# Kernel optimization log

Hardware: AMD Instinct MI355X
Metric: run time of the kernel (lower is better)

## Reference

```python
import jax, jax.numpy as jnp
import numpy as np

TOP_K = 2

def setup_inputs() -> dict:
    key = jax.random.key(0)
    ks = jax.random.split(key, 7)
    B, L, D, H, E, S = 2, 2048, 1024, 512, 16, 2048
    s = lambda fan_in: (1.0 / np.sqrt(fan_in)).astype(np.float32)
    return {
        "x": jax.random.normal(ks[0], (B, L, D), jnp.float32),
        "gate_w": jax.random.normal(ks[1], (E, D), jnp.float32) * s(D),
        "w1": jax.random.normal(ks[2], (E, H, D), jnp.float32) * s(D),
        "w2": jax.random.normal(ks[3], (E, D, H), jnp.float32) * s(H),
        "sfc1": jax.random.normal(ks[4], (S, D), jnp.float32) * s(D),
        "sfc2": jax.random.normal(ks[5], (S, D), jnp.float32) * s(D),
        "sfc3": jax.random.normal(ks[6], (D, S), jnp.float32) * s(S),
    }

def reference(x, gate_w, w1, w2, sfc1, sfc2, sfc3):
    B, L, D = x.shape
    E = gate_w.shape[0]
    # shared expert: SwiGLU MLP
    shared = jnp.einsum("bls,ds->bld", jax.nn.silu(jnp.einsum("bld,sd->bls", x, sfc1)) * jnp.einsum("bld,sd->bls", x, sfc2), sfc3)
    # router: top-k over gate logits, softmax over selected logits only
    logits = jnp.einsum("bld,ed->ble", x, gate_w)
    top_w, top_idx = jax.lax.top_k(logits, TOP_K)           # [B,L,K]
    top_w = jax.nn.softmax(top_w, axis=-1)
    xf = x.reshape(-1, D)                                    # [T,D]
    T = xf.shape[0]
    idx = top_idx.reshape(T, TOP_K)
    wk = top_w.reshape(T, TOP_K)
    # dense combine weights [T,E]: routing weight where selected, else 0
    dispatch = jnp.zeros((T, E), xf.dtype).at[jnp.arange(T)[:, None], idx].add(wk)
    # all-expert dense compute, combined with dispatch weights (avoids [T,E,D])
    h = jax.nn.silu(jnp.einsum("td,ehd->teh", xf, w1))       # [T,E,H]
    moe = jnp.einsum("teh,te,edh->td", h, dispatch, w2)      # [T,D]
    return moe.reshape(B, L, D) + shared
```

## Files before the change

kernel.cpp:

```cpp
#include <hip/hip_runtime.h>
#include <stdint.h>

#define T_TOK 4096
#define D_DIM 1024
#define H_DIM 512
#define E_NUM 16
#define S_DIM 2048

#define CAST2_BLOCKS 256
#define DUAL_BLOCKS 512
#define MOE1_TILES_MAX 80
#define SHOUT_BLOCKS 256

typedef __attribute__((ext_vector_type(8))) __bf16 bf16x8;
typedef __attribute__((ext_vector_type(4))) float f32x4;

__device__ __forceinline__ uint16_t f2bf(float f) {
  uint32_t u = __float_as_uint(f);
  u += 0x7fffu + ((u >> 16) & 1u);
  return (uint16_t)(u >> 16);
}

__device__ __forceinline__ float bf2f(uint16_t u) {
  return __uint_as_float(((uint32_t)u) << 16);
}

__device__ __forceinline__ float silu_f(float v) {
  return v / (1.f + __expf(-v));
}

#define N4_X (T_TOK * D_DIM / 4)
#define N4_S (S_DIM * D_DIM / 4)
#define N4_W (E_NUM * H_DIM * D_DIM / 4)
#define N4_P1 (N4_X + 2 * N4_S + N4_W)
#define N4_GW (E_NUM * D_DIM / 4)
#define N4_P2 (N4_S + N4_W)

__global__ __launch_bounds__(256) void k_cast1(
    const float* __restrict__ x, const float* __restrict__ sfc1,
    const float* __restrict__ sfc2, const float* __restrict__ w1,
    const float* __restrict__ gw,
    uint16_t* __restrict__ xb, uint16_t* __restrict__ s1b,
    uint16_t* __restrict__ s2b, uint16_t* __restrict__ w1b,
    float4* __restrict__ gwT4) {
  int i = blockIdx.x * 256 + threadIdx.x;
  if (i >= N4_P1) {
    int t = i - N4_P1;
    if (t < N4_GW) {
      int k4 = t & (D_DIM / 4 - 1);
      int e = t >> 8;
      gwT4[(size_t)k4 * E_NUM + e] = ((const float4*)(gw + (size_t)e * D_DIM))[k4];
    }
    return;
  }
  const float* src; uint16_t* dst; int off;
  if (i < N4_X)                  { src = x;    dst = xb;  off = 0; }
  else if (i < N4_X + N4_S)      { src = sfc1; dst = s1b; off = N4_X; }
  else if (i < N4_X + 2 * N4_S)  { src = sfc2; dst = s2b; off = N4_X + N4_S; }
  else                           { src = w1;   dst = w1b; off = N4_X + 2 * N4_S; }
  int j = i - off;
  float4 v = ((const float4*)src)[j];
  ushort4 o;
  o.x = f2bf(v.x); o.y = f2bf(v.y); o.z = f2bf(v.z); o.w = f2bf(v.w);
  ((ushort4*)dst)[j] = o;
}

__global__ __launch_bounds__(256) void k_router(
    const float* __restrict__ x, const float4* __restrict__ gwT4,
    int* __restrict__ top_idx, float* __restrict__ top_w) {
  const int wid = threadIdx.x >> 6, lane = threadIdx.x & 63;
  const int t = blockIdx.x * 4 + wid;
  const int e = lane & 15, q = lane >> 4;
  const float4* xr4 = (const float4*)(x + (size_t)t * D_DIM) + q * 64;
  const float4* g4 = gwT4 + (size_t)q * 64 * E_NUM + e;
  float acc = 0.f;
#pragma unroll 8
  for (int i = 0; i < 64; i++) {
    float4 xv = xr4[i];
    float4 gv = g4[(size_t)i * E_NUM];
    acc += xv.x * gv.x + xv.y * gv.y + xv.z * gv.z + xv.w * gv.w;
  }
  acc += __shfl_xor(acc, 16, 64);
  acc += __shfl_xor(acc, 32, 64);
  float v1 = acc; int i1 = e;
#pragma unroll
  for (int off = 1; off < 16; off <<= 1) {
    float ov = __shfl_xor(v1, off, 64);
    int oi = __shfl_xor(i1, off, 64);
    if (ov > v1 || (ov == v1 && oi < i1)) { v1 = ov; i1 = oi; }
  }
  float v2 = (e == i1) ? -1e30f : acc; int i2 = e;
#pragma unroll
  for (int off = 1; off < 16; off <<= 1) {
    float ov = __shfl_xor(v2, off, 64);
    int oi = __shfl_xor(i2, off, 64);
    if (ov > v2 || (ov == v2 && oi < i2)) { v2 = ov; i2 = oi; }
  }
  if (lane == 0) {
    float w0 = 1.f / (1.f + __expf(v2 - v1));
    top_idx[t * 2] = i1; top_idx[t * 2 + 1] = i2;
    top_w[t * 2] = w0;  top_w[t * 2 + 1] = 1.f - w0;
  }
}

__global__ __launch_bounds__(256) void k_sort(
    const int* __restrict__ top_idx, const float* __restrict__ top_w,
    int* __restrict__ offsets, int* __restrict__ tile_e,
    int* __restrict__ tile_m, int* __restrict__ tile_cnt,
    int* __restrict__ slot_token, float* __restrict__ slot_w,
    int* __restrict__ slot_of) {
  __shared__ int h[E_NUM];
  __shared__ int offs[E_NUM + 1];
  int tid = threadIdx.x;
  if (tid < E_NUM) h[tid] = 0;
  __syncthreads();
  for (int i = tid; i < 2 * T_TOK; i += 256) atomicAdd(&h[top_idx[i]], 1);
  __syncthreads();
  if (tid == 0) {
    int s = 0;
    for (int e = 0; e < E_NUM; e++) { offs[e] = s; s += h[e]; }
    offs[E_NUM] = s;
    int cnt = 0;
    for (int e = 0; e < E_NUM; e++)
      for (int m0 = 0; m0 < h[e]; m0 += 128) { tile_e[cnt] = e; tile_m[cnt] = m0; cnt++; }
    tile_cnt[0] = cnt;
    for (int e = 0; e <= E_NUM; e++) offsets[e] = offs[e];
  }
  __syncthreads();
  if (tid < E_NUM) h[tid] = offs[tid];
  __syncthreads();
  for (int i = tid; i < 2 * T_TOK; i += 256) {
    int e = top_idx[i];
    int slot = atomicAdd(&h[e], 1);
    slot_token[slot] = i >> 1;
    slot_w[slot] = top_w[i];
    slot_of[i] = slot;
  }
}

__global__ __launch_bounds__(256) void k_stage1(
    const uint16_t* __restrict__ xb, const uint16_t* __restrict__ b1,
    const uint16_t* __restrict__ b2, uint16_t* __restrict__ hs,
    const uint16_t* __restrict__ w1b, const int* __restrict__ offsets,
    const int* __restrict__ slot_token, const int* __restrict__ tile_e,
    const int* __restrict__ tile_m, const int* __restrict__ tile_cnt,
    uint16_t* __restrict__ hbuf,
    const float* __restrict__ sfc3, const float* __restrict__ w2,
    uint16_t* __restrict__ s3b, uint16_t* __restrict__ w2b) {
  __shared__ uint16_t smem[6 * 4096];
  const int bid = blockIdx.x;
  const int tid = threadIdx.x, lane = tid & 63, wid = tid >> 6;
  const int wm = wid >> 1, wn = wid & 1;
  const int r = lane & 15, q = lane >> 4;
  const int row0 = tid >> 2, col8 = (tid & 3) * 8;
  const int st0 = tid * 8, st1 = 2048 + tid * 8;

  if (bid < CAST2_BLOCKS) {
    for (int i = bid * 256 + tid; i < N4_P2; i += CAST2_BLOCKS * 256) {
      const float* src; uint16_t* dst; int j;
      if (i < N4_S) { src = sfc3; dst = s3b; j = i; }
      else          { src = w2;   dst = w2b; j = i - N4_S; }
      float4 v = ((const float4*)src)[j];
      ushort4 o;
      o.x = f2bf(v.x); o.y = f2bf(v.y); o.z = f2bf(v.z); o.w = f2bf(v.w);
      ((ushort4*)dst)[j] = o;
    }
    return;
  }

  if (bid < CAST2_BLOCKS + DUAL_BLOCKS) {
    const int b = bid - CAST2_BLOCKS;
    const int bm0 = (b & 31) * 128, bn0 = (b >> 5) * 128;
    uint16_t* sA = smem;
    uint16_t* sB1 = smem + 8192;
    uint16_t* sB2 = smem + 16384;
    f32x4 acc1[4][4], acc2[4][4];
#pragma unroll
    for (int i = 0; i < 4; i++)
#pragma unroll
      for (int j = 0; j < 4; j++) {
        acc1[i][j] = (f32x4){0.f, 0.f, 0.f, 0.f};
        acc2[i][j] = (f32x4){0.f, 0.f, 0.f, 0.f};
      }
    const uint16_t* ga0 = xb + (size_t)(bm0 + row0) * D_DIM + col8;
    const uint16_t* ga1 = ga0 + 64 * D_DIM;
    const uint16_t* gb10 = b1 + (size_t)(bn0 + row0) * D_DIM + col8;
    const uint16_t* gb11 = gb10 + 64 * D_DIM;
    const uint16_t* gb20 = b2 + (size_t)(bn0 + row0) * D_DIM + col8;
    const uint16_t* gb21 = gb20 + 64 * D_DIM;

    uint4 pA0, pA1, pB10, pB11, pB20, pB21;
    pA0 = *(const uint4*)ga0;   pA1 = *(const uint4*)ga1;
    pB10 = *(const uint4*)gb10; pB11 = *(const uint4*)gb11;
    pB20 = *(const uint4*)gb20; pB21 = *(const uint4*)gb21;
    ga0 += 32; ga1 += 32; gb10 += 32; gb11 += 32; gb20 += 32; gb21 += 32;
    *(uint4*)(sA + st0) = pA0;   *(uint4*)(sA + st1) = pA1;
    *(uint4*)(sB1 + st0) = pB10; *(uint4*)(sB1 + st1) = pB11;
    *(uint4*)(sB2 + st0) = pB20; *(uint4*)(sB2 + st1) = pB21;
    __syncthreads();

    int cur = 0;
    for (int kt = 32; kt < D_DIM; kt += 32) {
      pA0 = *(const uint4*)ga0;   pA1 = *(const uint4*)ga1;
      pB10 = *(const uint4*)gb10; pB11 = *(const uint4*)gb11;
      pB20 = *(const uint4*)gb20; pB21 = *(const uint4*)gb21;
      ga0 += 32; ga1 += 32; gb10 += 32; gb11 += 32; gb20 += 32; gb21 += 32;
      {
        const uint16_t* A = sA + cur * 4096;
        const uint16_t* B1 = sB1 + cur * 4096;
        const uint16_t* B2 = sB2 + cur * 4096;
        bf16x8 a[4];
#pragma unroll
        for (int i = 0; i < 4; i++)
          a[i] = *(const bf16x8*)(A + (wm * 64 + i * 16 + r) * 32 + q * 8);
#pragma unroll
        for (int j = 0; j < 4; j++) {
          bf16x8 b = *(const bf16x8*)(B1 + (wn * 64 + j * 16 + r) * 32 + q * 8);
#pragma unroll
          for (int i = 0; i < 4; i++)
            acc1[i][j] = __builtin_amdgcn_mfma_f32_16x16x32_bf16(a[i], b, acc1[i][j], 0, 0, 0);
        }
#pragma unroll
        for (int j = 0; j < 4; j++) {
          bf16x8 b = *(const bf16x8*)(B2 + (wn * 64 + j * 16 + r) * 32 + q * 8);
#pragma unroll
          for (int i = 0; i < 4; i++)
            acc2[i][j] = __builtin_amdgcn_mfma_f32_16x16x32_bf16(a[i], b, acc2[i][j], 0, 0, 0);
        }
      }
      int nxt = cur ^ 1;
      *(uint4*)(sA + nxt * 4096 + st0) = pA0;   *(uint4*)(sA + nxt * 4096 + st1) = pA1;
      *(uint4*)(sB1 + nxt * 4096 + st0) = pB10; *(uint4*)(sB1 + nxt * 4096 + st1) = pB11;
      *(uint4*)(sB2 + nxt * 4096 + st0) = pB20; *(uint4*)(sB2 + nxt * 4096 + st1) = pB21;
      __syncthreads();
      cur = nxt;
    }
    {
      const uint16_t* A = sA + cur * 4096;
      const uint16_t* B1 = sB1 + cur * 4096;
      const uint16_t* B2 = sB2 + cur * 4096;
      bf16x8 a[4];
#pragma unroll
      for (int i = 0; i < 4; i++)
        a[i] = *(const bf16x8*)(A + (wm * 64 + i * 16 + r) * 32 + q * 8);
#pragma unroll
      for (int j = 0; j < 4; j++) {
        bf16x8 b = *(const bf16x8*)(B1 + (wn * 64 + j * 16 + r) * 32 + q * 8);
#pragma unroll
        for (int i = 0; i < 4; i++)
          acc1[i][j] = __builtin_amdgcn_mfma_f32_16x16x32_bf16(a[i], b, acc1[i][j], 0, 0, 0);
      }
#pragma unroll
      for (int j = 0; j < 4; j++) {
        bf16x8 b = *(const bf16x8*)(B2 + (wn * 64 + j * 16 + r) * 32 + q * 8);
#pragma unroll
        for (int i = 0; i < 4; i++)
          acc2[i][j] = __builtin_amdgcn_mfma_f32_16x16x32_bf16(a[i], b, acc2[i][j], 0, 0, 0);
      }
    }
#pragma unroll
    for (int i = 0; i < 4; i++)
#pragma unroll
      for (int j = 0; j < 4; j++)
#pragma unroll
        for (int rr = 0; rr < 4; rr++) {
          int row = bm0 + wm * 64 + i * 16 + q * 4 + rr;
          int col = bn0 + wn * 64 + j * 16 + r;
          hs[(size_t)row * S_DIM + col] = f2bf(silu_f(acc1[i][j][rr]) * acc2[i][j][rr]);
        }
  } else {
    int idx = bid - CAST2_BLOCKS - DUAL_BLOCKS;
    int t = idx >> 2;
    if (t >= tile_cnt[0]) return;
    const int n0 = (idx & 3) * 128;
    const int e = tile_e[t], m0 = tile_m[t];
    const int base = offsets[e];
    const int ne = offsets[e + 1] - base;
    uint16_t* sA = smem;
    uint16_t* sB = smem + 8192;
    f32x4 acc[4][4];
#pragma unroll
    for (int i = 0; i < 4; i++)
#pragma unroll
      for (int j = 0; j < 4; j++) acc[i][j] = (f32x4){0.f, 0.f, 0.f, 0.f};
    const int e0 = min(m0 + row0, ne - 1);
    const int e1 = min(m0 + row0 + 64, ne - 1);
    const uint16_t* ga0 = xb + (size_t)slot_token[base + e0] * D_DIM + col8;
    const uint16_t* ga1 = xb + (size_t)slot_token[base + e1] * D_DIM + col8;
    const uint16_t* wbase = w1b + (size_t)e * H_DIM * D_DIM;
    const uint16_t* gb0 = wbase + (size_t)(n0 + row0) * D_DIM + col8;
    const uint16_t* gb1 = gb0 + 64 * D_DIM;

    uint4 pA0, pA1, pB0, pB1;
    pA0 = *(const uint4*)ga0; pA1 = *(const uint4*)ga1;
    pB0 = *(const uint4*)gb0; pB1 = *(const uint4*)gb1;
    ga0 += 32; ga1 += 32; gb0 += 32; gb1 += 32;
    *(uint4*)(sA + st0) = pA0; *(uint4*)(sA + st1) = pA1;
    *(uint4*)(sB + st0) = pB0; *(uint4*)(sB + st1) = pB1;
    __syncthreads();

    int cur = 0;
    for (int kt = 32; kt < D_DIM; kt += 32) {
      pA0 = *(const uint4*)ga0; pA1 = *(const uint4*)ga1;
      pB0 = *(const uint4*)gb0; pB1 = *(const uint4*)gb1;
      ga0 += 32; ga1 += 32; gb0 += 32; gb1 += 32;
      {
        const uint16_t* A = sA + cur * 4096;
        const uint16_t* B = sB + cur * 4096;
        bf16x8 a[4], bb[4];
#pragma unroll
        for (int i = 0; i < 4; i++)
          a[i] = *(const bf16x8*)(A + (wm * 64 + i * 16 + r) * 32 + q * 8);
#pragma unroll
        for (int j = 0; j < 4; j++)
          bb[j] = *(const bf16x8*)(B + (wn * 64 + j * 16 + r) * 32 + q * 8);
#pragma unroll
        for (int i = 0; i < 4; i++)
#pragma unroll
          for (int j = 0; j < 4; j++)
            acc[i][j] = __builtin_amdgcn_mfma_f32_16x16x32_bf16(a[i], bb[j], acc[i][j], 0, 0, 0);
      }
      int nxt = cur ^ 1;
      *(uint4*)(sA + nxt * 4096 + st0) = pA0; *(uint4*)(sA + nxt * 4096 + st1) = pA1;
      *(uint4*)(sB + nxt * 4096 + st0) = pB0; *(uint4*)(sB + nxt * 4096 + st1) = pB1;
      __syncthreads();
      cur = nxt;
    }
    {
      const uint16_t* A = sA + cur * 4096;
      const uint16_t* B = sB + cur * 4096;
      bf16x8 a[4], bb[4];
#pragma unroll
      for (int i = 0; i < 4; i++)
        a[i] = *(const bf16x8*)(A + (wm * 64 + i * 16 + r) * 32 + q * 8);
#pragma unroll
      for (int j = 0; j < 4; j++)
        bb[j] = *(const bf16x8*)(B + (wn * 64 + j * 16 + r) * 32 + q * 8);
#pragma unroll
      for (int i = 0; i < 4; i++)
#pragma unroll
        for (int j = 0; j < 4; j++)
          acc[i][j] = __builtin_amdgcn_mfma_f32_16x16x32_bf16(a[i], bb[j], acc[i][j], 0, 0, 0);
    }
#pragma unroll
    for (int i = 0; i < 4; i++)
#pragma unroll
      for (int j = 0; j < 4; j++)
#pragma unroll
        for (int rr = 0; rr < 4; rr++) {
          int ent = m0 + wm * 64 + i * 16 + q * 4 + rr;
          if (ent < ne) {
            int col = n0 + wn * 64 + j * 16 + r;
            hbuf[(size_t)(base + ent) * H_DIM + col] = f2bf(silu_f(acc[i][j][rr]));
          }
        }
  }
}

__global__ __launch_bounds__(256) void k_stage2(
    const uint16_t* __restrict__ hsb, const uint16_t* __restrict__ sfc3b,
    float* __restrict__ out, const uint16_t* __restrict__ hbuf,
    const uint16_t* __restrict__ w2b, const int* __restrict__ offsets,
    const float* __restrict__ slot_w, const int* __restrict__ tile_e,
    const int* __restrict__ tile_m, const int* __restrict__ tile_cnt,
    uint16_t* __restrict__ slot_out) {
  __shared__ uint16_t smem[4 * 4096];
  const int bid = blockIdx.x;
  const int tid = threadIdx.x, lane = tid & 63, wid = tid >> 6;
  const int wm = wid >> 1, wn = wid & 1;
  const int r = lane & 15, q = lane >> 4;
  const int row0 = tid >> 2, col8 = (tid & 3) * 8;
  const int st0 = tid * 8, st1 = 2048 + tid * 8;
  uint16_t* sA = smem;
  uint16_t* sB = smem + 8192;

  f32x4 acc[4][4];
#pragma unroll
  for (int i = 0; i < 4; i++)
#pragma unroll
    for (int j = 0; j < 4; j++) acc[i][j] = (f32x4){0.f, 0.f, 0.f, 0.f};

  const uint16_t *ga0, *ga1, *gb0, *gb1;
  int kiters;
  int bm0 = 0, bn0 = 0, base = 0, ne = 0, m0 = 0, n0 = 0;
  bool is_shout = (bid < SHOUT_BLOCKS);
  if (is_shout) {
    bm0 = (bid & 31) * 128; bn0 = (bid >> 5) * 128;
    ga0 = hsb + (size_t)(bm0 + row0) * S_DIM + col8;
    ga1 = ga0 + (size_t)64 * S_DIM;
    gb0 = sfc3b + (size_t)(bn0 + row0) * S_DIM + col8;
    gb1 = gb0 + (size_t)64 * S_DIM;
    kiters = S_DIM / 32;
  } else {
    int idx = bid - SHOUT_BLOCKS;
    int t = idx >> 3;
    if (t >= tile_cnt[0]) return;
    n0 = (idx & 7) * 128;
    int e = tile_e[t]; m0 = tile_m[t];
    base = offsets[e];
    ne = offsets[e + 1] - base;
    const int e0 = min(m0 + row0, ne - 1);
    const int e1 = min(m0 + row0 + 64, ne - 1);
    ga0 = hbuf + (size_t)(base + e0) * H_DIM + col8;
    ga1 = hbuf + (size_t)(base + e1) * H_DIM + col8;
    const uint16_t* wbase = w2b + (size_t)e * D_DIM * H_DIM;
    gb0 = wbase + (size_t)(n0 + row0) * H_DIM + col8;
    gb1 = gb0 + 64 * H_DIM;
    kiters = H_DIM / 32;
  }

  uint4 pA0, pA1, pB0, pB1;
  pA0 = *(const uint4*)ga0; pA1 = *(const uint4*)ga1;
  pB0 = *(const uint4*)gb0; pB1 = *(const uint4*)gb1;
  ga0 += 32; ga1 += 32; gb0 += 32; gb1 += 32;
  *(uint4*)(sA + st0) = pA0; *(uint4*)(sA + st1) = pA1;
  *(uint4*)(sB + st0) = pB0; *(uint4*)(sB + st1) = pB1;
  __syncthreads();

  int cur = 0;
  for (int kt = 1; kt <= kiters; kt++) {
    if (kt < kiters) {
      pA0 = *(const uint4*)ga0; pA1 = *(const uint4*)ga1;
      pB0 = *(const uint4*)gb0; pB1 = *(const uint4*)gb1;
      ga0 += 32; ga1 += 32; gb0 += 32; gb1 += 32;
    }
    {
      const uint16_t* A = sA + cur * 4096;
      const uint16_t* B = sB + cur * 4096;
      bf16x8 a[4], bb[4];
#pragma unroll
      for (int i = 0; i < 4; i++)
        a[i] = *(const bf16x8*)(A + (wm * 64 + i * 16 + r) * 32 + q * 8);
#pragma unroll
      for (int j = 0; j < 4; j++)
        bb[j] = *(const bf16x8*)(B + (wn * 64 + j * 16 + r) * 32 + q * 8);
#pragma unroll
      for (int i = 0; i < 4; i++)
#pragma unroll
        for (int j = 0; j < 4; j++)
          acc[i][j] = __builtin_amdgcn_mfma_f32_16x16x32_bf16(a[i], bb[j], acc[i][j], 0, 0, 0);
    }
    if (kt < kiters) {
      int nxt = cur ^ 1;
      *(uint4*)(sA + nxt * 4096 + st0) = pA0; *(uint4*)(sA + nxt * 4096 + st1) = pA1;
      *(uint4*)(sB + nxt * 4096 + st0) = pB0; *(uint4*)(sB + nxt * 4096 + st1) = pB1;
      __syncthreads();
      cur = nxt;
    }
  }

  if (is_shout) {
#pragma unroll
    for (int i = 0; i < 4; i++)
#pragma unroll
      for (int j = 0; j < 4; j++)
#pragma unroll
        for (int rr = 0; rr < 4; rr++) {
          int row = bm0 + wm * 64 + i * 16 + q * 4 + rr;
          int col = bn0 + wn * 64 + j * 16 + r;
          out[(size_t)row * D_DIM + col] = acc[i][j][rr];
        }
  } else {
#pragma unroll
    for (int i = 0; i < 4; i++) {
      int ent_base = m0 + wm * 64 + i * 16 + q * 4;
#pragma unroll
      for (int rr = 0; rr < 4; rr++) {
        int ent = ent_base + rr;
        if (ent < ne) {
          float w = slot_w[base + ent];
          uint16_t* orow = slot_out + (size_t)(base + ent) * D_DIM;
#pragma unroll
          for (int j = 0; j < 4; j++) {
            int col = n0 + wn * 64 + j * 16 + r;
            orow[col] = f2bf(w * acc[i][j][rr]);
          }
        }
      }
    }
  }
}

__global__ __launch_bounds__(256) void k_combine(
    const uint16_t* __restrict__ slot_out, const int* __restrict__ slot_of,
    float* __restrict__ out) {
  int t = blockIdx.x;
  int c = threadIdx.x;
  int s0 = slot_of[t * 2], s1 = slot_of[t * 2 + 1];
  ushort4 a = ((const ushort4*)(slot_out + (size_t)s0 * D_DIM))[c];
  ushort4 b = ((const ushort4*)(slot_out + (size_t)s1 * D_DIM))[c];
  float4* po = (float4*)(out + (size_t)t * D_DIM) + c;
  float4 o = *po;
  o.x += bf2f(a.x) + bf2f(b.x);
  o.y += bf2f(a.y) + bf2f(b.y);
  o.z += bf2f(a.z) + bf2f(b.z);
  o.w += bf2f(a.w) + bf2f(b.w);
  *po = o;
}

extern "C" void kernel_launch(void* const* d_in, const int* in_sizes, int n_in,
                              void* d_out, int out_size, void* d_ws, size_t ws_size,
                              hipStream_t stream) {
  const float* x     = (const float*)d_in[0];
  const float* gatew = (const float*)d_in[1];
  const float* w1    = (const float*)d_in[2];
  const float* w2    = (const float*)d_in[3];
  const float* sfc1  = (const float*)d_in[4];
  const float* sfc2  = (const float*)d_in[5];
  const float* sfc3  = (const float*)d_in[6];
  float* out = (float*)d_out;

  uint8_t* ws = (uint8_t*)d_ws;
  size_t off = 0;
  auto alloc = [&](size_t bytes) {
    void* p = ws + off;
    off = (off + bytes + 255) & ~(size_t)255;
    return p;
  };
  uint16_t* xb    = (uint16_t*)alloc((size_t)T_TOK * D_DIM * 2);
  uint16_t* sfc1b = (uint16_t*)alloc((size_t)S_DIM * D_DIM * 2);
  uint16_t* sfc2b = (uint16_t*)alloc((size_t)S_DIM * D_DIM * 2);
  uint16_t* sfc3b = (uint16_t*)alloc((size_t)D_DIM * S_DIM * 2);
  uint16_t* w1b   = (uint16_t*)alloc((size_t)E_NUM * H_DIM * D_DIM * 2);
  uint16_t* w2b   = (uint16_t*)alloc((size_t)E_NUM * D_DIM * H_DIM * 2);
  uint16_t* hsb   = (uint16_t*)alloc((size_t)T_TOK * S_DIM * 2);
  uint16_t* hbuf  = (uint16_t*)alloc((size_t)2 * T_TOK * H_DIM * 2);
  uint16_t* slot_out = (uint16_t*)alloc((size_t)2 * T_TOK * D_DIM * 2);
  float4* gwT4    = (float4*)alloc((size_t)D_DIM / 4 * E_NUM * 16);
  int*   top_idx  = (int*)alloc((size_t)T_TOK * 2 * 4);
  float* top_w    = (float*)alloc((size_t)T_TOK * 2 * 4);
  int*   offsets  = (int*)alloc((E_NUM + 1) * 4);
  int*   tile_e   = (int*)alloc(MOE1_TILES_MAX * 4);
  int*   tile_m   = (int*)alloc(MOE1_TILES_MAX * 4);
  int*   tile_cnt = (int*)alloc(4);
  int*   slot_token = (int*)alloc((size_t)2 * T_TOK * 4);
  float* slot_w   = (float*)alloc((size_t)2 * T_TOK * 4);
  int*   slot_of  = (int*)alloc((size_t)2 * T_TOK * 4);

  k_cast1<<<(N4_P1 + N4_GW + 255) / 256, 256, 0, stream>>>(
      x, sfc1, sfc2, w1, gatew, xb, sfc1b, sfc2b, w1b, gwT4);
  k_router<<<T_TOK / 4, 256, 0, stream>>>(x, gwT4, top_idx, top_w);
  k_sort<<<1, 256, 0, stream>>>(top_idx, top_w, offsets, tile_e, tile_m,
                                tile_cnt, slot_token, slot_w, slot_of);
  k_stage1<<<CAST2_BLOCKS + DUAL_BLOCKS + MOE1_TILES_MAX * 4, 256, 0, stream>>>(
      xb, sfc1b, sfc2b, hsb, w1b, offsets, slot_token, tile_e, tile_m, tile_cnt,
      hbuf, sfc3, w2, sfc3b, w2b);
  k_stage2<<<SHOUT_BLOCKS + MOE1_TILES_MAX * 8, 256, 0, stream>>>(
      hsb, sfc3b, out, hbuf, w2b, offsets, slot_w, tile_e, tile_m, tile_cnt, slot_out);
  k_combine<<<T_TOK, 256, 0, stream>>>(slot_out, slot_of, out);
}
```

Baseline: 317.5 us.

## Fuse all weight casts with router into one kernel, drop gate transpose

Moves the sfc3/w2 bf16 casts out of stage1 into the first kernel and merges the router into that same launch as extra blocks. The router now reads gate weights directly in row layout instead of a transposed copy, which removes the transpose pass and its buffer. This drops one kernel launch and frees stage1 of cast blocks that competed with the GEMM tiles. In exchange, the casts of sfc3 and w2 no longer overlap with stage1 compute, and the router's gate-weight reads are strided per lane instead of coalesced.

Measured after the change: 352.3 us. +11.0%, slower.

```diff
diff --git a/kernel.cpp b/kernel.cpp
--- a/kernel.cpp
+++ b/kernel.cpp
@@ -7,7 +7,6 @@
 #define E_NUM 16
 #define S_DIM 2048
 
-#define CAST2_BLOCKS 256
 #define DUAL_BLOCKS 512
 #define MOE1_TILES_MAX 80
 #define SHOUT_BLOCKS 256
@@ -32,52 +31,47 @@
 #define N4_X (T_TOK * D_DIM / 4)
 #define N4_S (S_DIM * D_DIM / 4)
 #define N4_W (E_NUM * H_DIM * D_DIM / 4)
-#define N4_P1 (N4_X + 2 * N4_S + N4_W)
-#define N4_GW (E_NUM * D_DIM / 4)
-#define N4_P2 (N4_S + N4_W)
-
-__global__ __launch_bounds__(256) void k_cast1(
+#define N4_TOT (N4_X + 3 * N4_S + 2 * N4_W)
+#define CAST_BLOCKS (N4_TOT / 256)
+#define ROUTER_BLOCKS (T_TOK / 4)
+
+__global__ __launch_bounds__(256) void k_cast_router(
     const float* __restrict__ x, const float* __restrict__ sfc1,
-    const float* __restrict__ sfc2, const float* __restrict__ w1,
+    const float* __restrict__ sfc2, const float* __restrict__ sfc3,
+    const float* __restrict__ w1, const float* __restrict__ w2,
     const float* __restrict__ gw,
     uint16_t* __restrict__ xb, uint16_t* __restrict__ s1b,
-    uint16_t* __restrict__ s2b, uint16_t* __restrict__ w1b,
-    float4* __restrict__ gwT4) {
-  int i = blockIdx.x * 256 + threadIdx.x;
-  if (i >= N4_P1) {
-    int t = i - N4_P1;
-    if (t < N4_GW) {
-      int k4 = t & (D_DIM / 4 - 1);
-      int e = t >> 8;
-      gwT4[(size_t)k4 * E_NUM + e] = ((const float4*)(gw + (size_t)e * D_DIM))[k4];
-    }
+    uint16_t* __restrict__ s2b, uint16_t* __restrict__ s3b,
+    uint16_t* __restrict__ w1b, uint16_t* __restrict__ w2b,
+    int* __restrict__ top_idx, float* __restrict__ top_w) {
+  const int bid = blockIdx.x;
+  if (bid < CAST_BLOCKS) {
+    int i = bid * 256 + threadIdx.x;
+    const float* src; uint16_t* dst; int off;
+    if (i < N4_X)                    { src = x;    dst = xb;  off = 0; }
+    else if (i < N4_X + N4_S)        { src = sfc1; dst = s1b; off = N4_X; }
+    else if (i < N4_X + 2 * N4_S)    { src = sfc2; dst = s2b; off = N4_X + N4_S; }
+    else if (i < N4_X + 3 * N4_S)    { src = sfc3; dst = s3b; off = N4_X + 2 * N4_S; }
+    else if (i < N4_X + 3 * N4_S + N4_W) { src = w1; dst = w1b; off = N4_X + 3 * N4_S; }
+    else                             { src = w2;  dst = w2b; off = N4_X + 3 * N4_S + N4_W; }
+    int j = i - off;
+    float4 v = ((const float4*)src)[j];
+    ushort4 o;
+    o.x = f2bf(v.x); o.y = f2bf(v.y); o.z = f2bf(v.z); o.w = f2bf(v.w);
+    ((ushort4*)dst)[j] = o;
     return;
   }
-  const float* src; uint16_t* dst; int off;
-  if (i < N4_X)                  { src = x;    dst = xb;  off = 0; }
-  else if (i < N4_X + N4_S)      { src = sfc1; dst = s1b; off = N4_X; }
-  else if (i < N4_X + 2 * N4_S)  { src = sfc2; dst = s2b; off = N4_X + N4_S; }
-  else                           { src = w1;   dst = w1b; off = N4_X + 2 * N4_S; }
-  int j = i - off;
-  float4 v = ((const float4*)src)[j];
-  ushort4 o;
-  o.x = f2bf(v.x); o.y = f2bf(v.y); o.z = f2bf(v.z); o.w = f2bf(v.w);
-  ((ushort4*)dst)[j] = o;
-}
-
-__global__ __launch_bounds__(256) void k_router(
-    const float* __restrict__ x, const float4* __restrict__ gwT4,
-    int* __restrict__ top_idx, float* __restrict__ top_w) {
+  const int b = bid - CAST_BLOCKS;
   const int wid = threadIdx.x >> 6, lane = threadIdx.x & 63;
-  const int t = blockIdx.x * 4 + wid;
+  const int t = b * 4 + wid;
   const int e = lane & 15, q = lane >> 4;
   const float4* xr4 = (const float4*)(x + (size_t)t * D_DIM) + q * 64;
-  const float4* g4 = gwT4 + (size_t)q * 64 * E_NUM + e;
+  const float4* g4 = (const float4*)(gw + (size_t)e * D_DIM) + q * 64;
   float acc = 0.f;
 #pragma unroll 8
   for (int i = 0; i < 64; i++) {
     float4 xv = xr4[i];
-    float4 gv = g4[(size_t)i * E_NUM];
+    float4 gv = g4[i];
     acc += xv.x * gv.x + xv.y * gv.y + xv.z * gv.z + xv.w * gv.w;
   }
   acc += __shfl_xor(acc, 16, 64);
@@ -144,9 +138,7 @@
     const uint16_t* __restrict__ w1b, const int* __restrict__ offsets,
     const int* __restrict__ slot_token, const int* __restrict__ tile_e,
     const int* __restrict__ tile_m, const int* __restrict__ tile_cnt,
-    uint16_t* __restrict__ hbuf,
-    const float* __restrict__ sfc3, const float* __restrict__ w2,
-    uint16_t* __restrict__ s3b, uint16_t* __restrict__ w2b) {
+    uint16_t* __restrict__ hbuf) {
   __shared__ uint16_t smem[6 * 4096];
   const int bid = blockIdx.x;
   const int tid = threadIdx.x, lane = tid & 63, wid = tid >> 6;
@@ -155,22 +147,8 @@
   const int row0 = tid >> 2, col8 = (tid & 3) * 8;
   const int st0 = tid * 8, st1 = 2048 + tid * 8;
 
-  if (bid < CAST2_BLOCKS) {
-    for (int i = bid * 256 + tid; i < N4_P2; i += CAST2_BLOCKS * 256) {
-      const float* src; uint16_t* dst; int j;
-      if (i < N4_S) { src = sfc3; dst = s3b; j = i; }
-      else          { src = w2;   dst = w2b; j = i - N4_S; }
-      float4 v = ((const float4*)src)[j];
-      ushort4 o;
-      o.x = f2bf(v.x); o.y = f2bf(v.y); o.z = f2bf(v.z); o.w = f2bf(v.w);
-      ((ushort4*)dst)[j] = o;
-    }
-    return;
-  }
-
-  if (bid < CAST2_BLOCKS + DUAL_BLOCKS) {
-    const int b = bid - CAST2_BLOCKS;
-    const int bm0 = (b & 31) * 128, bn0 = (b >> 5) * 128;
+  if (bid < DUAL_BLOCKS) {
+    const int bm0 = (bid & 31) * 128, bn0 = (bid >> 5) * 128;
     uint16_t* sA = smem;
     uint16_t* sB1 = smem + 8192;
     uint16_t* sB2 = smem + 16384;
@@ -269,7 +247,7 @@
           hs[(size_t)row * S_DIM + col] = f2bf(silu_f(acc1[i][j][rr]) * acc2[i][j][rr]);
         }
   } else {
-    int idx = bid - CAST2_BLOCKS - DUAL_BLOCKS;
+    int idx = bid - DUAL_BLOCKS;
     int t = idx >> 2;
     if (t >= tile_cnt[0]) return;
     const int n0 = (idx & 3) * 128;
@@ -526,7 +504,6 @@
   uint16_t* hsb   = (uint16_t*)alloc((size_t)T_TOK * S_DIM * 2);
   uint16_t* hbuf  = (uint16_t*)alloc((size_t)2 * T_TOK * H_DIM * 2);
   uint16_t* slot_out = (uint16_t*)alloc((size_t)2 * T_TOK * D_DIM * 2);
-  float4* gwT4    = (float4*)alloc((size_t)D_DIM / 4 * E_NUM * 16);
   int*   top_idx  = (int*)alloc((size_t)T_TOK * 2 * 4);
   float* top_w    = (float*)alloc((size_t)T_TOK * 2 * 4);
   int*   offsets  = (int*)alloc((E_NUM + 1) * 4);
@@ -537,14 +514,13 @@
   float* slot_w   = (float*)alloc((size_t)2 * T_TOK * 4);
   int*   slot_of  = (int*)alloc((size_t)2 * T_TOK * 4);
 
-  k_cast1<<<(N4_P1 + N4_GW + 255) / 256, 256, 0, stream>>>(
-      x, sfc1, sfc2, w1, gatew, xb, sfc1b, sfc2b, w1b, gwT4);
-  k_router<<<T_TOK / 4, 256, 0, stream>>>(x, gwT4, top_idx, top_w);
+  k_cast_router<<<CAST_BLOCKS + ROUTER_BLOCKS, 256, 0, stream>>>(
+      x, sfc1, sfc2, sfc3, w1, w2, gatew,
+      xb, sfc1b, sfc2b, sfc3b, w1b, w2b, top_idx, top_w);
   k_sort<<<1, 256, 0, stream>>>(top_idx, top_w, offsets, tile_e, tile_m,
                                 tile_cnt, slot_token, slot_w, slot_of);
-  k_stage1<<<CAST2_BLOCKS + DUAL_BLOCKS + MOE1_TILES_MAX * 4, 256, 0, stream>>>(
-      xb, sfc1b, sfc2b, hsb, w1b, offsets, slot_token, tile_e, tile_m, tile_cnt,
-      hbuf, sfc3, w2, sfc3b, w2b);
+  k_stage1<<<DUAL_BLOCKS + MOE1_TILES_MAX * 4, 256, 0, stream>>>(
+      xb, sfc1b, sfc2b, hsb, w1b, offsets, slot_token, tile_e, tile_m, tile_cnt, hbuf);
   k_stage2<<<SHOUT_BLOCKS + MOE1_TILES_MAX * 8, 256, 0, stream>>>(
       hsb, sfc3b, out, hbuf, w2b, offsets, slot_w, tile_e, tile_m, tile_cnt, slot_out);
   k_combine<<<T_TOK, 256, 0, stream>>>(slot_out, slot_of, out);
```
